# Performance work log

Measured on AMD Instinct MI355X. Metric: run time of the kernel, lower is better.

The kernel has to match this reference:

```python
import jax, jax.numpy as jnp
import numpy as np

H, W = 64, 64          # self.shape = (W, H) = (64, 64)
REG_MAX = 16
TOPK = 4

def _dwconv(y, w, b):
    # y: (N, L, C) -> depthwise 3x3 conv on (N, C, H, W) -> (N, L, C)
    N, L, C = y.shape
    img = jnp.transpose(y, (0, 2, 1)).reshape(N, C, H, W)
    out = jax.lax.conv_general_dilated(
        img, w, (1, 1), ((1, 1), (1, 1)),
        dimension_numbers=('NCHW', 'OIHW', 'NCHW'), feature_group_count=C)
    out = out + b[None, :, None, None]
    return jnp.transpose(out.reshape(N, C, H * W), (0, 2, 1))

def _mlp(x, fc1_w, fc1_b, dw1_w, dw1_b, fc2_w, fc2_b, dw2_w, dw2_b, fc3_w, fc3_b):
    h = x @ fc1_w.T + fc1_b
    h = jax.nn.gelu(_dwconv(h, dw1_w, dw1_b), approximate=False)  # torch nn.GELU is exact erf
    h = h @ fc2_w.T + fc2_b
    h = jax.nn.gelu(_dwconv(h, dw2_w, dw2_b), approximate=False)
    return h @ fc3_w.T + fc3_b

def setup_inputs() -> dict:
    key = jax.random.key(0)
    ks = iter(jax.random.split(key, 16))
    d = {}
    d['x'] = jax.random.normal(next(ks), (1, 32, H * W, 256), dtype=jnp.float32)
    for p in ('c_', 'r_'):
        out3 = 1 if p == 'c_' else 4 * (REG_MAX + 1)
        d[p + 'fc1_w'] = 0.02 * jax.random.normal(next(ks), (256, 256), dtype=jnp.float32)
        d[p + 'fc1_b'] = jnp.zeros((256,), jnp.float32)
        d[p + 'dw1_w'] = 0.3 * jax.random.normal(next(ks), (256, 1, 3, 3), dtype=jnp.float32)
        d[p + 'dw1_b'] = jnp.zeros((256,), jnp.float32)
        d[p + 'fc2_w'] = 0.02 * jax.random.normal(next(ks), (256, 256), dtype=jnp.float32)
        d[p + 'fc2_b'] = jnp.zeros((256,), jnp.float32)
        d[p + 'dw2_w'] = 0.3 * jax.random.normal(next(ks), (256, 1, 3, 3), dtype=jnp.float32)
        d[p + 'dw2_b'] = jnp.zeros((256,), jnp.float32)
        d[p + 'fc3_w'] = 0.02 * jax.random.normal(next(ks), (out3, 256), dtype=jnp.float32)
        d[p + 'fc3_b'] = jnp.zeros((out3,), jnp.float32)
    d['rc1_w'] = 0.1 * jax.random.normal(next(ks), (64, 4 * (TOPK + 1)), dtype=jnp.float32)
    d['rc1_b'] = jnp.zeros((64,), jnp.float32)
    d['rc2_w'] = 0.1 * jax.random.normal(next(ks), (1, 64), dtype=jnp.float32)
    d['rc2_b'] = jnp.zeros((1,), jnp.float32)
    return d

def reference(x,
              c_fc1_w, c_fc1_b, c_dw1_w, c_dw1_b, c_fc2_w, c_fc2_b, c_dw2_w, c_dw2_b, c_fc3_w, c_fc3_b,
              r_fc1_w, r_fc1_b, r_dw1_w, r_dw1_b, r_fc2_w, r_fc2_b, r_dw2_w, r_dw2_b, r_fc3_w, r_fc3_b,
              rc1_w, rc1_b, rc2_w, rc2_b):
    xs = x[0]                                   # (N, L, C)
    N = xs.shape[0]
    reg_pred = _mlp(xs, r_fc1_w, r_fc1_b, r_dw1_w, r_dw1_b, r_fc2_w, r_fc2_b,
                    r_dw2_w, r_dw2_b, r_fc3_w, r_fc3_b)  # (N, L, 4*(reg_max+1))
    prob = jax.nn.softmax(
        jnp.transpose(reg_pred, (0, 2, 1)).reshape(N, 4, REG_MAX + 1, H, W), axis=2)
    pt = jnp.transpose(prob, (0, 1, 3, 4, 2))   # (N,4,H,W,reg_max+1)
    topk, _ = jax.lax.top_k(pt, TOPK)           # (N,4,H,W,topk), sorted desc like torch
    stat = jnp.concatenate([topk, topk.mean(axis=-1, keepdims=True)], axis=-1)
    stat = jnp.transpose(stat, (0, 1, 4, 2, 3)).reshape(N, 4 * (TOPK + 1), H, W)
    q = jax.nn.relu(jnp.einsum('nchw,oc->nohw', stat, rc1_w) + rc1_b[None, :, None, None])
    q = jax.nn.sigmoid(jnp.einsum('nchw,oc->nohw', q, rc2_w) + rc2_b[None, :, None, None])
    cls = _mlp(xs, c_fc1_w, c_fc1_b, c_dw1_w, c_dw1_b, c_fc2_w, c_fc2_b,
               c_dw2_w, c_dw2_b, c_fc3_w, c_fc3_b)      # (N, L, 1)
    cls = jax.nn.sigmoid(jnp.transpose(cls, (0, 2, 1)).reshape(N, 1, H, W)) * q
    proj = jnp.arange(REG_MAX + 1, dtype=reg_pred.dtype)  # linspace(0, reg_max, reg_max+1)
    dist = jax.nn.softmax(reg_pred.reshape(-1, REG_MAX + 1), axis=1) @ proj
    boxes = dist.reshape(N, H, W, 4) / REG_MAX
    return cls, boxes, reg_pred.reshape(N, H, W, 4 * (REG_MAX + 1))
```

## Files before the change

### kernel.cpp

```cpp
#include <hip/hip_runtime.h>
#include <hip/hip_bf16.h>

typedef __bf16 bf16x8 __attribute__((ext_vector_type(8)));
typedef float f32x4 __attribute__((ext_vector_type(4)));
typedef float f32x2 __attribute__((ext_vector_type(2)));

__device__ __forceinline__ float bf2f(unsigned short b) {
  unsigned int u = ((unsigned int)b) << 16;
  return __builtin_bit_cast(float, u);
}
__device__ __forceinline__ unsigned short f2bf(float f) {
  unsigned int u = __builtin_bit_cast(unsigned int, f);
  unsigned int r = u + 0x7fffu + ((u >> 16) & 1u);
  return (unsigned short)(r >> 16);
}
__device__ __forceinline__ f32x2 unpack2(unsigned int u) {
  f32x2 r;
  r.x = __builtin_bit_cast(float, u << 16);
  r.y = __builtin_bit_cast(float, u & 0xffff0000u);
  return r;
}

__device__ __forceinline__ void gload16(const void* g, void* l) {
  typedef __attribute__((address_space(1))) const void* gp_t;
  typedef __attribute__((address_space(3))) void* lp_t;
  __builtin_amdgcn_global_load_lds((gp_t)g, (lp_t)l, 16, 0, 0);
}

__device__ __forceinline__ f32x2 gelu2(f32x2 x) {
  f32x2 z = x * 0.70710678118654752440f;
  f32x2 az; az.x = fabsf(z.x); az.y = fabsf(z.y);
  f32x2 t;
  t.x = __builtin_amdgcn_rcpf(__builtin_fmaf(0.3275911f, az.x, 1.0f));
  t.y = __builtin_amdgcn_rcpf(__builtin_fmaf(0.3275911f, az.y, 1.0f));
  f32x2 y = t * (0.254829592f + t * (-0.284496736f + t * (1.421413741f +
            t * (-1.453152027f + t * 1.061405429f))));
  f32x2 zz = z * z;
  f32x2 e; e.x = __expf(-zz.x); e.y = __expf(-zz.y);
  f32x2 ec = y * e;
  f32x2 d = 0.5f - 0.5f * ec;
  f32x2 ph;
  ph.x = 0.5f + __builtin_copysignf(d.x, z.x);
  ph.y = 0.5f + __builtin_copysignf(d.y, z.y);
  return x * ph;
}

__global__ __launch_bounds__(256) void cvt_x(const float* __restrict__ in,
                                             unsigned short* __restrict__ out) {
  long i = ((long)blockIdx.x * 256 + threadIdx.x) * 8;
  float4 a = *(const float4*)(in + i);
  float4 b = *(const float4*)(in + i + 4);
  __align__(16) unsigned short o[8];
  o[0] = f2bf(a.x); o[1] = f2bf(a.y); o[2] = f2bf(a.z); o[3] = f2bf(a.w);
  o[4] = f2bf(b.x); o[5] = f2bf(b.y); o[6] = f2bf(b.z); o[7] = f2bf(b.w);
  *(uint4*)(out + i) = *(uint4*)o;
}

__global__ __launch_bounds__(256) void prep_all(
    const float* __restrict__ c1w, const float* __restrict__ r1w,
    const float* __restrict__ c2w, const float* __restrict__ r2w,
    const float* __restrict__ c3w, const float* __restrict__ r3w, const float* __restrict__ r3b,
    const float* __restrict__ c1b, const float* __restrict__ r1b,
    const float* __restrict__ c2b, const float* __restrict__ r2b,
    const float* __restrict__ d1wc, const float* __restrict__ d1bc,
    const float* __restrict__ d1wr, const float* __restrict__ d1br,
    const float* __restrict__ d2wc, const float* __restrict__ d2bc,
    const float* __restrict__ d2wr, const float* __restrict__ d2br,
    unsigned short* __restrict__ w1cat, unsigned short* __restrict__ w2cat,
    unsigned short* __restrict__ c3wb, unsigned short* __restrict__ wr3pad,
    float* __restrict__ br3pad, float* __restrict__ b1cat, float* __restrict__ b2cat,
    float* __restrict__ wd1, float* __restrict__ bd1,
    float* __restrict__ wd2, float* __restrict__ bd2) {
  int i = blockIdx.x * 256 + threadIdx.x;
  {
    int which = i >> 16, j = i & 65535;
    float v = (which == 0) ? c1w[j] : (which == 1) ? r1w[j] : (which == 2) ? c2w[j] : r2w[j];
    unsigned short* dst = (which < 2) ? (w1cat + which * 65536) : (w2cat + (which - 2) * 65536);
    dst[j] = f2bf(v);
  }
  if (i < 32768) {
    int r = i >> 8, c = i & 255;
    wr3pad[i] = (r < 68) ? f2bf(r3w[r * 256 + c]) : (unsigned short)0;
    if (i < 128) br3pad[i] = (i < 68) ? r3b[i] : 0.f;
  }
  if (i < 256) c3wb[i] = f2bf(c3w[i]);
  if (i < 4608) {
    int tap = i >> 9, ch = i & 511, cc = ch & 255;
    wd1[i] = (ch < 256) ? d1wc[cc * 9 + tap] : d1wr[cc * 9 + tap];
    wd2[i] = (ch < 256) ? d2wc[cc * 9 + tap] : d2wr[cc * 9 + tap];
  }
  if (i < 512) {
    bd1[i] = (i < 256) ? d1bc[i] : d1br[i & 255];
    bd2[i] = (i < 256) ? d2bc[i] : d2br[i & 255];
    b1cat[i] = (i < 256) ? c1b[i] : r1b[i & 255];
    b2cat[i] = (i < 256) ? c2b[i] : r2b[i & 255];
  }
}

__global__ __launch_bounds__(256, 3) void gemm_glds(
    const unsigned short* __restrict__ A, int lda, int zAoff,
    const unsigned short* __restrict__ W, int zWoff,
    const float* __restrict__ bias, int zBoff,
    unsigned short* __restrict__ Out, int ldo, int zOoff, int lnN) {
  __shared__ unsigned short lds[2][8192];
  const int z = blockIdx.z;
  const unsigned short* Az = A + (long)z * zAoff;
  const unsigned short* Wz = W + (long)z * zWoff;
  const float* biasz = bias + z * zBoff;
  unsigned short* Outz = Out + (long)z * zOoff;

  const int nwg = gridDim.x;
  const int bid = blockIdx.x;
  const int wg = (bid & 7) * (nwg >> 3) + (bid >> 3);
  const int mtile = wg >> lnN;
  const int ntile = wg & ((1 << lnN) - 1);
  const long row0 = (long)mtile * 128;
  const int col0 = ntile * 128;

  const int tid = threadIdx.x;
  const int lane = tid & 63;
  const int wid = tid >> 6;
  const int wr = (wid >> 1) * 64;
  const int wc = (wid & 1) * 64;
  const int rr = lane & 15;
  const int gk = lane >> 4;
  const int swz = (rr >> 1) & 3;

  const int srow_l = (wid << 4) + (lane >> 2);
  const int sgl = lane & 3;

  f32x4 acc[4][4] = {};

  auto stage = [&](int buf, int k0) {
    #pragma unroll
    for (int j = 0; j < 4; j++) {
      const int slotbase = j * 256 + (wid << 6);
      unsigned short* ldst = &lds[buf][slotbase * 8];
      const int row = (j & 1) * 64 + srow_l;
      const int g = sgl ^ ((row >> 1) & 3);
      const unsigned short* src;
      if (j < 2) src = Az + (row0 + row) * (long)lda + k0 + g * 8;
      else       src = Wz + (long)(col0 + row) * 256 + k0 + g * 8;
      gload16(src, ldst);
    }
  };

  stage(0, 0);
  #pragma unroll
  for (int ks = 0; ks < 8; ks++) {
    if (ks < 7) {
      stage((ks + 1) & 1, (ks + 1) * 32);
      asm volatile("s_waitcnt vmcnt(4)" ::: "memory");
    } else {
      asm volatile("s_waitcnt vmcnt(0)" ::: "memory");
    }
    __builtin_amdgcn_s_barrier();
    asm volatile("" ::: "memory");
    const unsigned short* buf = lds[ks & 1];
    bf16x8 af[4], bf[4];
    #pragma unroll
    for (int mi = 0; mi < 4; mi++)
      af[mi] = __builtin_bit_cast(bf16x8,
          *(const uint4*)&buf[(wr + mi * 16 + rr) * 32 + ((gk ^ swz) * 8)]);
    #pragma unroll
    for (int ni = 0; ni < 4; ni++)
      bf[ni] = __builtin_bit_cast(bf16x8,
          *(const uint4*)&buf[4096 + (wc + ni * 16 + rr) * 32 + ((gk ^ swz) * 8)]);
    #pragma unroll
    for (int mi = 0; mi < 4; mi++)
      #pragma unroll
      for (int ni = 0; ni < 4; ni++)
        acc[mi][ni] = __builtin_amdgcn_mfma_f32_16x16x32_bf16(af[mi], bf[ni], acc[mi][ni], 0, 0, 0);
    asm volatile("" ::: "memory");
    __builtin_amdgcn_s_barrier();
  }

  #pragma unroll
  for (int mi = 0; mi < 4; mi++) {
    const int rbase = wr + mi * 16 + (lane >> 4) * 4;
    #pragma unroll
    for (int ni = 0; ni < 4; ni++) {
      const int c_ = wc + ni * 16 + (lane & 15);
      const float bv = biasz[col0 + c_];
      #pragma unroll
      for (int r = 0; r < 4; r++) {
        Outz[(row0 + rbase + r) * (long)ldo + col0 + c_] = f2bf(acc[mi][ni][r] + bv);
      }
    }
  }
}

__global__ __launch_bounds__(256) void dwconv_gelu2(
    const unsigned short* __restrict__ In,
    const float* __restrict__ Wt, const float* __restrict__ Bt,
    unsigned short* __restrict__ Out) {
  int t = blockIdx.x * 256 + threadIdx.x;
  int g = t & 63;
  int p = t >> 6;
  int n = p >> 11;
  int h = (p >> 5) & 63;
  int w0 = (p & 31) * 2;
  int cbase = g << 3;
  f32x2 accA[4], accB[4];
  {
    float4 b0 = *(const float4*)(Bt + cbase);
    float4 b1 = *(const float4*)(Bt + cbase + 4);
    accA[0].x = b0.x; accA[0].y = b0.y; accA[1].x = b0.z; accA[1].y = b0.w;
    accA[2].x = b1.x; accA[2].y = b1.y; accA[3].x = b1.z; accA[3].y = b1.w;
    #pragma unroll
    for (int i = 0; i < 4; i++) accB[i] = accA[i];
  }
  #pragma unroll
  for (int dy = -1; dy <= 1; dy++) {
    int hh = h + dy;
    if (hh < 0 || hh > 63) continue;
    const float* wb = Wt + ((dy + 1) * 3) * 512 + cbase;
    f32x2 wt0[4], wt1[4], wt2[4];
    {
      float4 a0 = *(const float4*)(wb);        float4 a1 = *(const float4*)(wb + 4);
      float4 b0 = *(const float4*)(wb + 512);  float4 b1 = *(const float4*)(wb + 516);
      float4 c0 = *(const float4*)(wb + 1024); float4 c1 = *(const float4*)(wb + 1028);
      wt0[0].x = a0.x; wt0[0].y = a0.y; wt0[1].x = a0.z; wt0[1].y = a0.w;
      wt0[2].x = a1.x; wt0[2].y = a1.y; wt0[3].x = a1.z; wt0[3].y = a1.w;
      wt1[0].x = b0.x; wt1[0].y = b0.y; wt1[1].x = b0.z; wt1[1].y = b0.w;
      wt1[2].x = b1.x; wt1[2].y = b1.y; wt1[3].x = b1.z; wt1[3].y = b1.w;
      wt2[0].x = c0.x; wt2[0].y = c0.y; wt2[1].x = c0.z; wt2[1].y = c0.w;
      wt2[2].x = c1.x; wt2[2].y = c1.y; wt2[3].x = c1.z; wt2[3].y = c1.w;
    }
    const long rowtok = (long)(((n << 6) + hh) << 6);
    if (w0 > 0) {
      uint4 v = *(const uint4*)(In + (rowtok + w0 - 1) * 512 + cbase);
      unsigned int u[4] = {v.x, v.y, v.z, v.w};
      #pragma unroll
      for (int i = 0; i < 4; i++) { f32x2 f = unpack2(u[i]); accA[i] += f * wt0[i]; }
    }
    {
      uint4 v = *(const uint4*)(In + (rowtok + w0) * 512 + cbase);
      unsigned int u[4] = {v.x, v.y, v.z, v.w};
      #pragma unroll
      for (int i = 0; i < 4; i++) { f32x2 f = unpack2(u[i]); accA[i] += f * wt1[i]; accB[i] += f * wt0[i]; }
    }
    {
      uint4 v = *(const uint4*)(In + (rowtok + w0 + 1) * 512 + cbase);
      unsigned int u[4] = {v.x, v.y, v.z, v.w};
      #pragma unroll
      for (int i = 0; i < 4; i++) { f32x2 f = unpack2(u[i]); accA[i] += f * wt2[i]; accB[i] += f * wt1[i]; }
    }
    if (w0 < 62) {
      uint4 v = *(const uint4*)(In + (rowtok + w0 + 2) * 512 + cbase);
      unsigned int u[4] = {v.x, v.y, v.z, v.w};
      #pragma unroll
      for (int i = 0; i < 4; i++) { f32x2 f = unpack2(u[i]); accB[i] += f * wt2[i]; }
    }
  }
  long mA = (long)(((n << 6) + h) << 6) + w0;
  __align__(16) unsigned short ov[8];
  #pragma unroll
  for (int i = 0; i < 4; i++) {
    f32x2 gA = gelu2(accA[i]);
    ov[2 * i] = f2bf(gA.x); ov[2 * i + 1] = f2bf(gA.y);
  }
  *(uint4*)(Out + mA * 512 + cbase) = *(uint4*)ov;
  #pragma unroll
  for (int i = 0; i < 4; i++) {
    f32x2 gB = gelu2(accB[i]);
    ov[2 * i] = f2bf(gB.x); ov[2 * i + 1] = f2bf(gB.y);
  }
  *(uint4*)(Out + (mA + 1) * 512 + cbase) = *(uint4*)ov;
}

__global__ __launch_bounds__(256) void cls_dot(
    const unsigned short* __restrict__ G2,
    const unsigned short* __restrict__ Wc3,
    const float* __restrict__ bc3,
    float* __restrict__ cls_logit) {
  int lane = threadIdx.x & 63;
  int wid = threadIdx.x >> 6;
  long m = (long)blockIdx.x * 4 + wid;
  const unsigned short* row = G2 + m * 512;
  ushort4 a = *(const ushort4*)(row + lane * 4);
  ushort4 wv = *(const ushort4*)(Wc3 + lane * 4);
  float s = bf2f(a.x) * bf2f(wv.x) + bf2f(a.y) * bf2f(wv.y) +
            bf2f(a.z) * bf2f(wv.z) + bf2f(a.w) * bf2f(wv.w);
  #pragma unroll
  for (int off = 32; off > 0; off >>= 1) s += __shfl_down(s, off);
  if (lane == 0) cls_logit[m] = s + bc3[0];
}

__global__ __launch_bounds__(256) void post_kernel(
    const unsigned short* __restrict__ RP,
    const float* __restrict__ cls_logit,
    const float* __restrict__ rc1_w, const float* __restrict__ rc1_b,
    const float* __restrict__ rc2_w, const float* __restrict__ rc2_b,
    float* __restrict__ out_cls, float* __restrict__ out_boxes, float* __restrict__ out_reg) {
  int m = blockIdx.x * 256 + threadIdx.x;
  const unsigned short* rp = RP + (long)m * 128;
  float stat[20];
  #pragma unroll
  for (int s = 0; s < 4; s++) {
    float v[17];
    float mx = -1e30f;
    #pragma unroll
    for (int i = 0; i < 17; i++) {
      v[i] = bf2f(rp[s * 17 + i]);
      out_reg[(long)m * 68 + s * 17 + i] = v[i];
      mx = fmaxf(mx, v[i]);
    }
    float sum = 0.f;
    #pragma unroll
    for (int i = 0; i < 17; i++) { v[i] = __expf(v[i] - mx); sum += v[i]; }
    float inv = 1.f / sum;
    float dist = 0.f;
    #pragma unroll
    for (int i = 0; i < 17; i++) { v[i] *= inv; dist += v[i] * (float)i; }
    out_boxes[(long)m * 4 + s] = dist * 0.0625f;
    float tk[4];
    #pragma unroll
    for (int t = 0; t < 4; t++) {
      float bm = v[0]; int bi = 0;
      #pragma unroll
      for (int i = 1; i < 17; i++) {
        if (v[i] > bm) { bm = v[i]; bi = i; }
      }
      tk[t] = bm;
      #pragma unroll
      for (int i = 0; i < 17; i++)
        if (i == bi) v[i] = -1.f;
    }
    stat[s * 5 + 0] = tk[0]; stat[s * 5 + 1] = tk[1];
    stat[s * 5 + 2] = tk[2]; stat[s * 5 + 3] = tk[3];
    stat[s * 5 + 4] = 0.25f * (tk[0] + tk[1] + tk[2] + tk[3]);
  }
  float z = 0.f;
  #pragma unroll
  for (int o = 0; o < 64; o++) {
    float q = rc1_b[o];
    #pragma unroll
    for (int c = 0; c < 20; c++) q += rc1_w[o * 20 + c] * stat[c];
    q = fmaxf(q, 0.f);
    z += q * rc2_w[o];
  }
  z += rc2_b[0];
  float q2 = 1.f / (1.f + __expf(-z));
  float cl = 1.f / (1.f + __expf(-cls_logit[m]));
  out_cls[m] = cl * q2;
}

extern "C" void kernel_launch(void* const* d_in, const int* in_sizes, int n_in,
                              void* d_out, int out_size, void* d_ws, size_t ws_size,
                              hipStream_t stream) {
  const float* x       = (const float*)d_in[0];
  const float* c_fc1_w = (const float*)d_in[1];
  const float* c_fc1_b = (const float*)d_in[2];
  const float* c_dw1_w = (const float*)d_in[3];
  const float* c_dw1_b = (const float*)d_in[4];
  const float* c_fc2_w = (const float*)d_in[5];
  const float* c_fc2_b = (const float*)d_in[6];
  const float* c_dw2_w = (const float*)d_in[7];
  const float* c_dw2_b = (const float*)d_in[8];
  const float* c_fc3_w = (const float*)d_in[9];
  const float* c_fc3_b = (const float*)d_in[10];
  const float* r_fc1_w = (const float*)d_in[11];
  const float* r_fc1_b = (const float*)d_in[12];
  const float* r_dw1_w = (const float*)d_in[13];
  const float* r_dw1_b = (const float*)d_in[14];
  const float* r_fc2_w = (const float*)d_in[15];
  const float* r_fc2_b = (const float*)d_in[16];
  const float* r_dw2_w = (const float*)d_in[17];
  const float* r_dw2_b = (const float*)d_in[18];
  const float* r_fc3_w = (const float*)d_in[19];
  const float* r_fc3_b = (const float*)d_in[20];
  const float* rc1_w   = (const float*)d_in[21];
  const float* rc1_b   = (const float*)d_in[22];
  const float* rc2_w   = (const float*)d_in[23];
  const float* rc2_b   = (const float*)d_in[24];

  char* ws = (char*)d_ws;
  unsigned short* Hbuf = (unsigned short*)ws;
  unsigned short* Gbuf = (unsigned short*)(ws + 134217728L);
  unsigned short* xb   = Gbuf;
  unsigned short* RP   = (unsigned short*)(ws + 268435456L);
  float* cls_logit     = (float*)(ws + 301989888L);
  char* wb             = ws + 302514176L;
  unsigned short* w1cat  = (unsigned short*)wb;
  unsigned short* w2cat  = w1cat + 131072;
  unsigned short* c3wb   = w2cat + 131072;
  unsigned short* wr3pad = c3wb + 256;
  float* br3pad = (float*)(wr3pad + 32768);
  float* b1cat  = br3pad + 128;
  float* b2cat  = b1cat + 512;
  float* wd1    = b2cat + 512;
  float* bd1    = wd1 + 4608;
  float* wd2    = bd1 + 512;
  float* bd2    = wd2 + 4608;

  prep_all<<<1024, 256, 0, stream>>>(
      c_fc1_w, r_fc1_w, c_fc2_w, r_fc2_w, c_fc3_w, r_fc3_w, r_fc3_b,
      c_fc1_b, r_fc1_b, c_fc2_b, r_fc2_b,
      c_dw1_w, c_dw1_b, r_dw1_w, r_dw1_b,
      c_dw2_w, c_dw2_b, r_dw2_w, r_dw2_b,
      w1cat, w2cat, c3wb, wr3pad, br3pad, b1cat, b2cat,
      wd1, bd1, wd2, bd2);
  cvt_x<<<16384, 256, 0, stream>>>(x, xb);

  gemm_glds<<<dim3(4096, 1, 1), 256, 0, stream>>>(
      xb, 256, 0, w1cat, 0, b1cat, 0, Hbuf, 512, 0, 2);
  dwconv_gelu2<<<16384, 256, 0, stream>>>(Hbuf, wd1, bd1, Gbuf);
  gemm_glds<<<dim3(2048, 1, 2), 256, 0, stream>>>(
      Gbuf, 512, 256, w2cat, 65536, b2cat, 256, Hbuf, 512, 256, 1);
  dwconv_gelu2<<<16384, 256, 0, stream>>>(Hbuf, wd2, bd2, Gbuf);
  cls_dot<<<32768, 256, 0, stream>>>(Gbuf, c3wb, c_fc3_b, cls_logit);
  gemm_glds<<<dim3(1024, 1, 1), 256, 0, stream>>>(
      Gbuf + 256, 512, 0, wr3pad, 0, br3pad, 0, RP, 128, 0, 0);
  float* out_cls   = (float*)d_out;
  float* out_boxes = out_cls + 131072;
  float* out_reg   = out_boxes + 524288;
  post_kernel<<<512, 256, 0, stream>>>(RP, cls_logit, rc1_w, rc1_b, rc2_w, rc2_b,
                                       out_cls, out_boxes, out_reg);
}
```

Measured before the change: 398.4 us.

## Fuse fp32-to-bf16 input conversion into first GEMM and widen dwconv tiles

The separate cvt_x pass is removed. The first GEMM is templated to load fp32 A tiles into registers, convert them to bf16 and write them to LDS after the MFMA step, which saves a full read and write of the converted activation buffer. The depthwise conv kernel now computes four horizontal outputs per thread instead of two, so neighbouring input columns are reused more and fewer threads are launched. The cost is more registers in both kernels and a software-managed A pipeline that needs the lgkmcnt waits to be correct.

```diff
diff --git a/kernel.cpp b/kernel.cpp
--- a/kernel.cpp
+++ b/kernel.cpp
@@ -43,17 +43,6 @@
   ph.x = 0.5f + __builtin_copysignf(d.x, z.x);
   ph.y = 0.5f + __builtin_copysignf(d.y, z.y);
   return x * ph;
-}
-
-__global__ __launch_bounds__(256) void cvt_x(const float* __restrict__ in,
-                                             unsigned short* __restrict__ out) {
-  long i = ((long)blockIdx.x * 256 + threadIdx.x) * 8;
-  float4 a = *(const float4*)(in + i);
-  float4 b = *(const float4*)(in + i + 4);
-  __align__(16) unsigned short o[8];
-  o[0] = f2bf(a.x); o[1] = f2bf(a.y); o[2] = f2bf(a.z); o[3] = f2bf(a.w);
-  o[4] = f2bf(b.x); o[5] = f2bf(b.y); o[6] = f2bf(b.z); o[7] = f2bf(b.w);
-  *(uint4*)(out + i) = *(uint4*)o;
 }
 
 __global__ __launch_bounds__(256) void prep_all(
@@ -97,14 +86,17 @@
   }
 }
 
+__global__ void __launch_bounds__(256, 3) gemm_common();
+template <bool AF32>
 __global__ __launch_bounds__(256, 3) void gemm_glds(
-    const unsigned short* __restrict__ A, int lda, int zAoff,
+    const void* __restrict__ Aptr, int lda, int zAoff,
     const unsigned short* __restrict__ W, int zWoff,
     const float* __restrict__ bias, int zBoff,
     unsigned short* __restrict__ Out, int ldo, int zOoff, int lnN) {
   __shared__ unsigned short lds[2][8192];
   const int z = blockIdx.z;
-  const unsigned short* Az = A + (long)z * zAoff;
+  const float* Azf = (const float*)Aptr + (long)z * zAoff;
+  const unsigned short* Azb = (const unsigned short*)Aptr + (long)z * zAoff;
   const unsigned short* Wz = W + (long)z * zWoff;
   const float* biasz = bias + z * zBoff;
   unsigned short* Outz = Out + (long)z * zOoff;
@@ -129,30 +121,73 @@
   const int srow_l = (wid << 4) + (lane >> 2);
   const int sgl = lane & 3;
 
+  float areg[2][8];
+
+  auto loadA = [&](int k0) {
+    if constexpr (AF32) {
+      #pragma unroll
+      for (int j = 0; j < 2; j++) {
+        const int row = j * 64 + srow_l;
+        const int gsw = sgl ^ ((row >> 1) & 3);
+        const float* src = Azf + (row0 + row) * (long)lda + k0 + gsw * 8;
+        *(float4*)&areg[j][0] = *(const float4*)src;
+        *(float4*)&areg[j][4] = *(const float4*)(src + 4);
+      }
+    }
+  };
+  auto writeA = [&](int buf) {
+    if constexpr (AF32) {
+      #pragma unroll
+      for (int j = 0; j < 2; j++) {
+        __align__(16) unsigned short tmp[8];
+        #pragma unroll
+        for (int q = 0; q < 8; q++) tmp[q] = f2bf(areg[j][q]);
+        const int slot = j * 256 + (wid << 6) + lane;
+        *(uint4*)&lds[buf][slot * 8] = *(uint4*)tmp;
+      }
+    }
+  };
+  auto stageA_gl = [&](int buf, int k0) {
+    if constexpr (!AF32) {
+      #pragma unroll
+      for (int j = 0; j < 2; j++) {
+        const int slotbase = j * 256 + (wid << 6);
+        const int row = j * 64 + srow_l;
+        const int gsw = sgl ^ ((row >> 1) & 3);
+        gload16(Azb + (row0 + row) * (long)lda + k0 + gsw * 8, &lds[buf][slotbase * 8]);
+      }
+    }
+  };
+  auto stageB = [&](int buf, int k0) {
+    #pragma unroll
+    for (int j = 2; j < 4; j++) {
+      const int slotbase = j * 256 + (wid << 6);
+      const int row = (j & 1) * 64 + srow_l;
+      const int gsw = sgl ^ ((row >> 1) & 3);
+      gload16(Wz + (long)(col0 + row) * 256 + k0 + gsw * 8, &lds[buf][slotbase * 8]);
+    }
+  };
+
   f32x4 acc[4][4] = {};
 
-  auto stage = [&](int buf, int k0) {
-    #pragma unroll
-    for (int j = 0; j < 4; j++) {
-      const int slotbase = j * 256 + (wid << 6);
-      unsigned short* ldst = &lds[buf][slotbase * 8];
-      const int row = (j & 1) * 64 + srow_l;
-      const int g = sgl ^ ((row >> 1) & 3);
-      const unsigned short* src;
-      if (j < 2) src = Az + (row0 + row) * (long)lda + k0 + g * 8;
-      else       src = Wz + (long)(col0 + row) * 256 + k0 + g * 8;
-      gload16(src, ldst);
-    }
-  };
-
-  stage(0, 0);
+  if constexpr (AF32) {
+    loadA(0); stageB(0, 0); writeA(0);
+  } else {
+    stageA_gl(0, 0); stageB(0, 0);
+  }
+
   #pragma unroll
   for (int ks = 0; ks < 8; ks++) {
     if (ks < 7) {
-      stage((ks + 1) & 1, (ks + 1) * 32);
-      asm volatile("s_waitcnt vmcnt(4)" ::: "memory");
+      if constexpr (AF32) {
+        loadA((ks + 1) * 32); stageB((ks + 1) & 1, (ks + 1) * 32);
+        asm volatile("s_waitcnt vmcnt(6) lgkmcnt(0)" ::: "memory");
+      } else {
+        stageA_gl((ks + 1) & 1, (ks + 1) * 32); stageB((ks + 1) & 1, (ks + 1) * 32);
+        asm volatile("s_waitcnt vmcnt(4)" ::: "memory");
+      }
     } else {
-      asm volatile("s_waitcnt vmcnt(0)" ::: "memory");
+      asm volatile("s_waitcnt vmcnt(0) lgkmcnt(0)" ::: "memory");
     }
     __builtin_amdgcn_s_barrier();
     asm volatile("" ::: "memory");
@@ -172,6 +207,7 @@
       for (int ni = 0; ni < 4; ni++)
         acc[mi][ni] = __builtin_amdgcn_mfma_f32_16x16x32_bf16(af[mi], bf[ni], acc[mi][ni], 0, 0, 0);
     asm volatile("" ::: "memory");
+    if (ks < 7) writeA((ks + 1) & 1);
     __builtin_amdgcn_s_barrier();
   }
 
@@ -190,83 +226,72 @@
   }
 }
 
-__global__ __launch_bounds__(256) void dwconv_gelu2(
+__global__ __launch_bounds__(256) void dwconv_gelu4(
     const unsigned short* __restrict__ In,
     const float* __restrict__ Wt, const float* __restrict__ Bt,
     unsigned short* __restrict__ Out) {
-  int t = blockIdx.x * 256 + threadIdx.x;
-  int g = t & 63;
-  int p = t >> 6;
-  int n = p >> 11;
-  int h = (p >> 5) & 63;
-  int w0 = (p & 31) * 2;
-  int cbase = g << 3;
-  f32x2 accA[4], accB[4];
+  const int t = blockIdx.x * 256 + threadIdx.x;
+  const int g = t & 63;
+  const int p = t >> 6;
+  const int n = p >> 10;
+  const int h = (p >> 4) & 63;
+  const int w0 = (p & 15) << 2;
+  const int cbase = g << 3;
+  f32x2 acc[4][4];
   {
     float4 b0 = *(const float4*)(Bt + cbase);
     float4 b1 = *(const float4*)(Bt + cbase + 4);
-    accA[0].x = b0.x; accA[0].y = b0.y; accA[1].x = b0.z; accA[1].y = b0.w;
-    accA[2].x = b1.x; accA[2].y = b1.y; accA[3].x = b1.z; accA[3].y = b1.w;
-    #pragma unroll
-    for (int i = 0; i < 4; i++) accB[i] = accA[i];
+    f32x2 bb[4];
+    bb[0].x = b0.x; bb[0].y = b0.y; bb[1].x = b0.z; bb[1].y = b0.w;
+    bb[2].x = b1.x; bb[2].y = b1.y; bb[3].x = b1.z; bb[3].y = b1.w;
+    #pragma unroll
+    for (int k = 0; k < 4; k++)
+      #pragma unroll
+      for (int i = 0; i < 4; i++) acc[k][i] = bb[i];
   }
   #pragma unroll
   for (int dy = -1; dy <= 1; dy++) {
-    int hh = h + dy;
+    const int hh = h + dy;
     if (hh < 0 || hh > 63) continue;
-    const float* wb = Wt + ((dy + 1) * 3) * 512 + cbase;
-    f32x2 wt0[4], wt1[4], wt2[4];
-    {
-      float4 a0 = *(const float4*)(wb);        float4 a1 = *(const float4*)(wb + 4);
-      float4 b0 = *(const float4*)(wb + 512);  float4 b1 = *(const float4*)(wb + 516);
-      float4 c0 = *(const float4*)(wb + 1024); float4 c1 = *(const float4*)(wb + 1028);
-      wt0[0].x = a0.x; wt0[0].y = a0.y; wt0[1].x = a0.z; wt0[1].y = a0.w;
-      wt0[2].x = a1.x; wt0[2].y = a1.y; wt0[3].x = a1.z; wt0[3].y = a1.w;
-      wt1[0].x = b0.x; wt1[0].y = b0.y; wt1[1].x = b0.z; wt1[1].y = b0.w;
-      wt1[2].x = b1.x; wt1[2].y = b1.y; wt1[3].x = b1.z; wt1[3].y = b1.w;
-      wt2[0].x = c0.x; wt2[0].y = c0.y; wt2[1].x = c0.z; wt2[1].y = c0.w;
-      wt2[2].x = c1.x; wt2[2].y = c1.y; wt2[3].x = c1.z; wt2[3].y = c1.w;
+    const float* wbase = Wt + ((dy + 1) * 3) * 512 + cbase;
+    f32x2 wt[3][4];
+    #pragma unroll
+    for (int j = 0; j < 3; j++) {
+      float4 a0 = *(const float4*)(wbase + j * 512);
+      float4 a1 = *(const float4*)(wbase + j * 512 + 4);
+      wt[j][0].x = a0.x; wt[j][0].y = a0.y; wt[j][1].x = a0.z; wt[j][1].y = a0.w;
+      wt[j][2].x = a1.x; wt[j][2].y = a1.y; wt[j][3].x = a1.z; wt[j][3].y = a1.w;
     }
     const long rowtok = (long)(((n << 6) + hh) << 6);
-    if (w0 > 0) {
-      uint4 v = *(const uint4*)(In + (rowtok + w0 - 1) * 512 + cbase);
-      unsigned int u[4] = {v.x, v.y, v.z, v.w};
-      #pragma unroll
-      for (int i = 0; i < 4; i++) { f32x2 f = unpack2(u[i]); accA[i] += f * wt0[i]; }
-    }
-    {
-      uint4 v = *(const uint4*)(In + (rowtok + w0) * 512 + cbase);
-      unsigned int u[4] = {v.x, v.y, v.z, v.w};
-      #pragma unroll
-      for (int i = 0; i < 4; i++) { f32x2 f = unpack2(u[i]); accA[i] += f * wt1[i]; accB[i] += f * wt0[i]; }
-    }
-    {
-      uint4 v = *(const uint4*)(In + (rowtok + w0 + 1) * 512 + cbase);
-      unsigned int u[4] = {v.x, v.y, v.z, v.w};
-      #pragma unroll
-      for (int i = 0; i < 4; i++) { f32x2 f = unpack2(u[i]); accA[i] += f * wt2[i]; accB[i] += f * wt1[i]; }
-    }
-    if (w0 < 62) {
-      uint4 v = *(const uint4*)(In + (rowtok + w0 + 2) * 512 + cbase);
-      unsigned int u[4] = {v.x, v.y, v.z, v.w};
-      #pragma unroll
-      for (int i = 0; i < 4; i++) { f32x2 f = unpack2(u[i]); accB[i] += f * wt2[i]; }
-    }
-  }
-  long mA = (long)(((n << 6) + h) << 6) + w0;
-  __align__(16) unsigned short ov[8];
-  #pragma unroll
-  for (int i = 0; i < 4; i++) {
-    f32x2 gA = gelu2(accA[i]);
-    ov[2 * i] = f2bf(gA.x); ov[2 * i + 1] = f2bf(gA.y);
-  }
-  *(uint4*)(Out + mA * 512 + cbase) = *(uint4*)ov;
-  #pragma unroll
-  for (int i = 0; i < 4; i++) {
-    f32x2 gB = gelu2(accB[i]);
-    ov[2 * i] = f2bf(gB.x); ov[2 * i + 1] = f2bf(gB.y);
-  }
-  *(uint4*)(Out + (mA + 1) * 512 + cbase) = *(uint4*)ov;
+    f32x2 f[6][4];
+    #pragma unroll
+    for (int d = 0; d < 6; d++) {
+      const int col = w0 - 1 + d;
+      uint4 v = {0u, 0u, 0u, 0u};
+      if (col >= 0 && col < 64)
+        v = *(const uint4*)(In + (rowtok + col) * 512 + cbase);
+      f[d][0] = unpack2(v.x); f[d][1] = unpack2(v.y);
+      f[d][2] = unpack2(v.z); f[d][3] = unpack2(v.w);
+    }
+    #pragma unroll
+    for (int k = 0; k < 4; k++)
+      #pragma unroll
+      for (int j = 0; j < 3; j++)
+        #pragma unroll
+        for (int i = 0; i < 4; i++)
+          acc[k][i] += f[k + j][i] * wt[j][i];
+  }
+  const long mbase = ((long)((n << 6) + h) << 6) + w0;
+  #pragma unroll
+  for (int k = 0; k < 4; k++) {
+    __align__(16) unsigned short ov[8];
+    #pragma unroll
+    for (int i = 0; i < 4; i++) {
+      f32x2 ge = gelu2(acc[k][i]);
+      ov[2 * i] = f2bf(ge.x); ov[2 * i + 1] = f2bf(ge.y);
+    }
+    *(uint4*)(Out + (mbase + k) * 512 + cbase) = *(uint4*)ov;
+  }
 }
 
 __global__ __launch_bounds__(256) void cls_dot(
@@ -378,7 +403,6 @@
   char* ws = (char*)d_ws;
   unsigned short* Hbuf = (unsigned short*)ws;
   unsigned short* Gbuf = (unsigned short*)(ws + 134217728L);
-  unsigned short* xb   = Gbuf;
   unsigned short* RP   = (unsigned short*)(ws + 268435456L);
   float* cls_logit     = (float*)(ws + 301989888L);
   char* wb             = ws + 302514176L;
@@ -401,16 +425,15 @@
       c_dw2_w, c_dw2_b, r_dw2_w, r_dw2_b,
       w1cat, w2cat, c3wb, wr3pad, br3pad, b1cat, b2cat,
       wd1, bd1, wd2, bd2);
-  cvt_x<<<16384, 256, 0, stream>>>(x, xb);
-
-  gemm_glds<<<dim3(4096, 1, 1), 256, 0, stream>>>(
-      xb, 256, 0, w1cat, 0, b1cat, 0, Hbuf, 512, 0, 2);
-  dwconv_gelu2<<<16384, 256, 0, stream>>>(Hbuf, wd1, bd1, Gbuf);
-  gemm_glds<<<dim3(2048, 1, 2), 256, 0, stream>>>(
+
+  gemm_glds<true><<<dim3(4096, 1, 1), 256, 0, stream>>>(
+      x, 256, 0, w1cat, 0, b1cat, 0, Hbuf, 512, 0, 2);
+  dwconv_gelu4<<<8192, 256, 0, stream>>>(Hbuf, wd1, bd1, Gbuf);
+  gemm_glds<false><<<dim3(2048, 1, 2), 256, 0, stream>>>(
       Gbuf, 512, 256, w2cat, 65536, b2cat, 256, Hbuf, 512, 256, 1);
-  dwconv_gelu2<<<16384, 256, 0, stream>>>(Hbuf, wd2, bd2, Gbuf);
+  dwconv_gelu4<<<8192, 256, 0, stream>>>(Hbuf, wd2, bd2, Gbuf);
   cls_dot<<<32768, 256, 0, stream>>>(Gbuf, c3wb, c_fc3_b, cls_logit);
-  gemm_glds<<<dim3(1024, 1, 1), 256, 0, stream>>>(
+  gemm_glds<false><<<dim3(1024, 1, 1), 256, 0, stream>>>(
       Gbuf + 256, 512, 0, wr3pad, 0, br3pad, 0, RP, 128, 0, 0);
   float* out_cls   = (float*)d_out;
   float* out_boxes = out_cls + 131072;
```

Measured after the change: 400.9 us. About the same (+0.6%).
